# Optimization experiments

Hardware: AMD Instinct MI355X
Metric: run time of the kernel (lower is better)

Reference implementation:

```python
import jax, jax.numpy as jnp
import numpy as np

ALPHA = 1e-4
BETA = 1.0
MAX_STD = 1000.0
MIN_STD = 1.0
B = 8192            # number of ragged segments (batch)
NUM_CLASSES = 2
P = 1_000_000       # size of penalized parameter vector


def setup_inputs() -> dict:
    key = jax.random.key(0)
    k1, k2, k3, k4 = jax.random.split(key, 4)
    # ragged lengths: alternate 1024 / 3072, exact total T = B * 2048
    lengths = np.where(np.arange(B) % 2 == 0, 1024, 3072).astype(np.int32)
    T = int(lengths.sum())  # 16_777_216
    seg = np.repeat(np.arange(B, dtype=np.int32), lengths)
    starts = np.concatenate([[0], np.cumsum(lengths)[:-1]])
    local = np.arange(T, dtype=np.int64) - np.repeat(starts, lengths)
    # get_x: positions (1..len)/len within each segment
    xpos = ((local + 1).astype(np.float64) / np.repeat(lengths, lengths)).astype(np.float32)
    return {
        "logits": jax.random.normal(k1, (B, NUM_CLASSES), jnp.float32),
        "labels": jax.random.randint(k2, (B,), 0, 2, jnp.int32),
        "attention_weights": jax.random.uniform(k3, (T,), jnp.float32),
        "params": jax.random.normal(k4, (P,), jnp.float32),
        "xpos": jnp.asarray(xpos),
        "segment_ids": jnp.asarray(seg),
        "lengths": jnp.asarray(lengths),
    }


def reference(logits, labels, attention_weights, params, xpos, segment_ids, lengths):
    nseg = logits.shape[0]
    lens_f = lengths.astype(jnp.float32)

    # CrossEntropyLoss (mean reduction)
    logp = jax.nn.log_softmax(logits, axis=-1)
    nll = -jnp.mean(jnp.take_along_axis(logp, labels[:, None].astype(jnp.int32), axis=1))

    # --- no-grad block: per-segment mean and ideal-gaussian target r ---
    w = jax.lax.stop_gradient(attention_weights)
    sum_w = jax.ops.segment_sum(w, segment_ids, num_segments=nseg)          # [B]
    mean = jax.ops.segment_sum(xpos * w, segment_ids, num_segments=nseg) / sum_w
    ideal_std = jnp.where(labels == 1, MIN_STD, MAX_STD) / lens_f           # [B]
    mu_t = mean[segment_ids]                                                # [T]
    std_t = ideal_std[segment_ids]                                          # [T]
    z = (xpos - mu_t) / std_t
    r_hat = jnp.exp(-0.5 * z * z) / (std_t * jnp.sqrt(2.0 * jnp.pi))        # normal pdf
    r_sum = jax.ops.segment_sum(r_hat, segment_ids, num_segments=nseg)
    r = r_hat / (r_sum[segment_ids] + 1e-6)
    r = jax.lax.stop_gradient(r)

    # L1 penalty on params
    penalty = ALPHA / 2 * jnp.abs(params).sum()

    # per-segment mean of squared diff, then mean over segments
    diff2 = (attention_weights - r) ** 2
    per_seg = jax.ops.segment_sum(diff2, segment_ids, num_segments=nseg) / lens_f
    awp = BETA / 2 * per_seg.mean()

    loss = nll + penalty + awp
    return jnp.stack([loss, nll])
```

## Files before the change

kernel.cpp:

```cpp
#include <hip/hip_runtime.h>


#define TPB 256
#define PARAM_BLOCKS 256
#define SEGS_PER_BLOCK 4

__device__ __forceinline__ void waveReduce3(float& a, float& b, float& c) {
  #pragma unroll
  for (int off = 32; off > 0; off >>= 1) {
    a += __shfl_xor(a, off, 64);
    b += __shfl_xor(b, off, 64);
    c += __shfl_xor(c, off, 64);
  }
}

__device__ __forceinline__ float blockReduceSum(float v, float* sm) {
  #pragma unroll
  for (int off = 32; off > 0; off >>= 1) v += __shfl_down(v, off, 64);
  const int lane = threadIdx.x & 63;
  const int wid  = threadIdx.x >> 6;
  if (lane == 0) sm[wid] = v;
  __syncthreads();
  float s = sm[0] + sm[1] + sm[2] + sm[3];
  __syncthreads();
  return s;
}

__global__ __launch_bounds__(TPB)
void scan_kernel(const int* __restrict__ lengths, int nseg,
                 int* __restrict__ starts) {
  __shared__ int wsum[4];
  const int t = threadIdx.x;
  const int per = (nseg + TPB - 1) / TPB;
  const int base = t * per;
  int local = 0;
  for (int j = 0; j < per; j++) {
    int idx = base + j;
    if (idx < nseg) local += lengths[idx];
  }
  const int lane = t & 63, wid = t >> 6;
  int incl = local;
  #pragma unroll
  for (int off = 1; off < 64; off <<= 1) {
    int n = __shfl_up(incl, off, 64);
    if (lane >= off) incl += n;
  }
  if (lane == 63) wsum[wid] = incl;
  __syncthreads();
  int wbase = 0;
  for (int i = 0; i < wid; i++) wbase += wsum[i];
  int run = wbase + incl - local;
  for (int j = 0; j < per; j++) {
    int idx = base + j;
    if (idx < nseg) { starts[idx] = run; run += lengths[idx]; }
  }
}

template <int NC>
__device__ __forceinline__ float seg_wave(const float4* __restrict__ w4,
                                          int start4, int len, int lab) {
  const int lane = threadIdx.x & 63;
  const float inv_len = 1.0f / (float)len;
  float4 wv[NC];
  float aw = 0.0f, axw = 0.0f, aww = 0.0f;
  #pragma unroll
  for (int k = 0; k < NC; k++) {
    const int vi = (k << 6) + lane;
    wv[k] = w4[start4 + vi];
    const int i0 = vi << 2;
    aw += wv[k].x + wv[k].y + wv[k].z + wv[k].w;
    axw = fmaf((float)(i0 + 1) * inv_len, wv[k].x, axw);
    axw = fmaf((float)(i0 + 2) * inv_len, wv[k].y, axw);
    axw = fmaf((float)(i0 + 3) * inv_len, wv[k].z, axw);
    axw = fmaf((float)(i0 + 4) * inv_len, wv[k].w, axw);
    aww = fmaf(wv[k].x, wv[k].x, aww);
    aww = fmaf(wv[k].y, wv[k].y, aww);
    aww = fmaf(wv[k].z, wv[k].z, aww);
    aww = fmaf(wv[k].w, wv[k].w, aww);
  }
  waveReduce3(aw, axw, aww);
  const float mean = axw / aw;
  const float invstd = (float)len * (lab == 1 ? 1.0f : 0.001f);
  const float rn = 0.39894228040143267f * invstd;
  float ar = 0.0f, awr = 0.0f, arr = 0.0f;
  #pragma unroll
  for (int k = 0; k < NC; k++) {
    const int i0 = ((k << 6) + lane) << 2;
    float z0 = ((float)(i0 + 1) * inv_len - mean) * invstd;
    float z1 = ((float)(i0 + 2) * inv_len - mean) * invstd;
    float z2 = ((float)(i0 + 3) * inv_len - mean) * invstd;
    float z3 = ((float)(i0 + 4) * inv_len - mean) * invstd;
    float r0 = __expf(-0.5f * z0 * z0) * rn;
    float r1 = __expf(-0.5f * z1 * z1) * rn;
    float r2 = __expf(-0.5f * z2 * z2) * rn;
    float r3 = __expf(-0.5f * z3 * z3) * rn;
    ar += r0 + r1 + r2 + r3;
    awr = fmaf(wv[k].x, r0, awr); awr = fmaf(wv[k].y, r1, awr);
    awr = fmaf(wv[k].z, r2, awr); awr = fmaf(wv[k].w, r3, awr);
    arr = fmaf(r0, r0, arr); arr = fmaf(r1, r1, arr);
    arr = fmaf(r2, r2, arr); arr = fmaf(r3, r3, arr);
  }
  waveReduce3(ar, awr, arr);
  const float rinv = 1.0f / (ar + 1e-6f);
  const float dsum = aww - 2.0f * rinv * awr + rinv * rinv * arr;
  return dsum * inv_len;
}

__device__ float seg_wave_generic(const float* __restrict__ w, int start,
                                  int len, int lab) {
  const int lane = threadIdx.x & 63;
  const float inv_len = 1.0f / (float)len;
  float aw = 0.0f, axw = 0.0f, aww = 0.0f;
  for (int i = lane; i < len; i += 64) {
    float wv = w[start + i];
    aw += wv;
    axw = fmaf((float)(i + 1) * inv_len, wv, axw);
    aww = fmaf(wv, wv, aww);
  }
  waveReduce3(aw, axw, aww);
  const float mean = axw / aw;
  const float invstd = (float)len * (lab == 1 ? 1.0f : 0.001f);
  const float rn = 0.39894228040143267f * invstd;
  float ar = 0.0f, awr = 0.0f, arr = 0.0f;
  for (int i = lane; i < len; i += 64) {
    float z = ((float)(i + 1) * inv_len - mean) * invstd;
    float rh = __expf(-0.5f * z * z) * rn;
    ar += rh;
    awr = fmaf(w[start + i], rh, awr);
    arr = fmaf(rh, rh, arr);
  }
  waveReduce3(ar, awr, arr);
  const float rinv = 1.0f / (ar + 1e-6f);
  const float dsum = aww - 2.0f * rinv * awr + rinv * rinv * arr;
  return dsum * inv_len;
}

__global__ __launch_bounds__(TPB)
void main_kernel(const float* __restrict__ attw, const float* __restrict__ params,
                 const float* __restrict__ logits, const int* __restrict__ labels,
                 const int* __restrict__ lengths, const int* __restrict__ starts,
                 int nseg, int P, float* __restrict__ partial) {
  __shared__ float sm[4];
  const int b = blockIdx.x;
  const int nsegblk = (nseg + SEGS_PER_BLOCK - 1) / SEGS_PER_BLOCK;
  if (b < nsegblk) {
    const int wid = threadIdx.x >> 6;
    const int seg = b * SEGS_PER_BLOCK + wid;
    if (seg < nseg) {
      const int len = lengths[seg];
      const int start = starts[seg];
      const int lab = labels[seg];
      float r;
      if (len == 1024 && (start & 3) == 0)
        r = seg_wave<4>((const float4*)attw, start >> 2, len, lab);
      else if (len == 3072 && (start & 3) == 0)
        r = seg_wave<12>((const float4*)attw, start >> 2, len, lab);
      else
        r = seg_wave_generic(attw, start, len, lab);
      if ((threadIdx.x & 63) == 0) partial[seg] = r;
    }
  } else if (b < nsegblk + PARAM_BLOCKS) {
    const int pb = b - nsegblk;
    const int P4 = P >> 2;
    const float4* p4 = (const float4*)params;
    float a = 0.0f;
    for (int i = pb * TPB + threadIdx.x; i < P4; i += PARAM_BLOCKS * TPB) {
      float4 v = p4[i];
      a += fabsf(v.x) + fabsf(v.y) + fabsf(v.z) + fabsf(v.w);
    }
    if (pb == 0 && threadIdx.x == 0)
      for (int i = P4 << 2; i < P; i++) a += fabsf(params[i]);
    float tot = blockReduceSum(a, sm);
    if (threadIdx.x == 0) partial[nseg + pb] = tot;
  } else {
    float acc = 0.0f;
    for (int s = threadIdx.x; s < nseg; s += TPB) {
      float l0 = logits[2 * s], l1 = logits[2 * s + 1];
      int lab = labels[s];
      float m = fmaxf(l0, l1);
      float lse = m + logf(expf(l0 - m) + expf(l1 - m));
      acc += (lab ? l1 : l0) - lse;
    }
    float tot = blockReduceSum(acc, sm);
    if (threadIdx.x == 0) partial[nseg + PARAM_BLOCKS] = tot;
  }
}

__global__ __launch_bounds__(TPB)
void finalize_kernel(const float* __restrict__ partial, int nseg,
                     float* __restrict__ out) {
  __shared__ float sm[8];
  float a_awp = 0.0f, a_abs = 0.0f;
  for (int i = threadIdx.x; i < nseg; i += TPB) a_awp += partial[i];
  for (int i = threadIdx.x; i < PARAM_BLOCKS; i += TPB) a_abs += partial[nseg + i];
  #pragma unroll
  for (int off = 32; off > 0; off >>= 1) {
    a_awp += __shfl_down(a_awp, off, 64);
    a_abs += __shfl_down(a_abs, off, 64);
  }
  const int lane = threadIdx.x & 63, wid = threadIdx.x >> 6;
  if (lane == 0) { sm[wid] = a_awp; sm[4 + wid] = a_abs; }
  __syncthreads();
  if (threadIdx.x == 0) {
    float s_awp = sm[0] + sm[1] + sm[2] + sm[3];
    float s_abs = sm[4] + sm[5] + sm[6] + sm[7];
    const float nll = -partial[nseg + PARAM_BLOCKS] / (float)nseg;
    const float penalty = 0.5f * 1e-4f * s_abs;
    const float awp = 0.5f * (s_awp / (float)nseg);
    out[0] = nll + penalty + awp;
    out[1] = nll;
  }
}

extern "C" void kernel_launch(void* const* d_in, const int* in_sizes, int n_in,
                              void* d_out, int out_size, void* d_ws, size_t ws_size,
                              hipStream_t stream) {
  const float* logits  = (const float*)d_in[0];
  const int*   labels  = (const int*)d_in[1];
  const float* attw    = (const float*)d_in[2];
  const float* params  = (const float*)d_in[3];
  const int*   lengths = (const int*)d_in[6];
  const int nseg = in_sizes[1];
  const int P    = in_sizes[3];

  int* starts = (int*)d_ws;
  size_t poff = ((size_t)nseg * sizeof(int) + 255) & ~(size_t)255;
  float* partial = (float*)((char*)d_ws + poff);
  float* out = (float*)d_out;

  const int nsegblk = (nseg + SEGS_PER_BLOCK - 1) / SEGS_PER_BLOCK;
  scan_kernel<<<1, TPB, 0, stream>>>(lengths, nseg, starts);
  main_kernel<<<nsegblk + PARAM_BLOCKS + 1, TPB, 0, stream>>>(
      attw, params, logits, labels, lengths, starts, nseg, P, partial);
  finalize_kernel<<<1, TPB, 0, stream>>>(partial, nseg, out);
}
```

Baseline: 211.3 us.

## Assign one block per segment instead of one wave per segment

Each segment is now processed by a full 256-thread block instead of a single 64-lane wave. Every wave partial is combined through shared memory, and each thread holds 1 or 3 float4 values rather than 4 or 12. The goal is to balance load between short and long segments, cut register pressure and give the memory system more parallelism. The z computation is also folded into a single FMA with precomputed constants. In exchange the kernel adds block barriers and launches four times as many blocks.

```diff
diff --git a/kernel.cpp b/kernel.cpp
--- a/kernel.cpp
+++ b/kernel.cpp
@@ -3,27 +3,30 @@
 
 #define TPB 256
 #define PARAM_BLOCKS 256
-#define SEGS_PER_BLOCK 4
-
-__device__ __forceinline__ void waveReduce3(float& a, float& b, float& c) {
+
+__device__ __forceinline__ void blockReduce3(float& a, float& b, float& c,
+                                             float* sm) {
   #pragma unroll
   for (int off = 32; off > 0; off >>= 1) {
     a += __shfl_xor(a, off, 64);
     b += __shfl_xor(b, off, 64);
     c += __shfl_xor(c, off, 64);
   }
+  const int lane = threadIdx.x & 63, wid = threadIdx.x >> 6;
+  if (lane == 0) { sm[wid] = a; sm[4 + wid] = b; sm[8 + wid] = c; }
+  __syncthreads();
+  a = sm[0] + sm[1] + sm[2] + sm[3];
+  b = sm[4] + sm[5] + sm[6] + sm[7];
+  c = sm[8] + sm[9] + sm[10] + sm[11];
 }
 
 __device__ __forceinline__ float blockReduceSum(float v, float* sm) {
   #pragma unroll
-  for (int off = 32; off > 0; off >>= 1) v += __shfl_down(v, off, 64);
-  const int lane = threadIdx.x & 63;
-  const int wid  = threadIdx.x >> 6;
+  for (int off = 32; off > 0; off >>= 1) v += __shfl_xor(v, off, 64);
+  const int lane = threadIdx.x & 63, wid = threadIdx.x >> 6;
   if (lane == 0) sm[wid] = v;
   __syncthreads();
-  float s = sm[0] + sm[1] + sm[2] + sm[3];
-  __syncthreads();
-  return s;
+  return sm[0] + sm[1] + sm[2] + sm[3];
 }
 
 __global__ __launch_bounds__(TPB)
@@ -57,15 +60,15 @@
 }
 
 template <int NC>
-__device__ __forceinline__ float seg_wave(const float4* __restrict__ w4,
-                                          int start4, int len, int lab) {
-  const int lane = threadIdx.x & 63;
+__device__ __forceinline__ float seg_body(const float4* __restrict__ w4,
+                                          int start4, int len, int lab,
+                                          float* sm) {
   const float inv_len = 1.0f / (float)len;
   float4 wv[NC];
   float aw = 0.0f, axw = 0.0f, aww = 0.0f;
   #pragma unroll
   for (int k = 0; k < NC; k++) {
-    const int vi = (k << 6) + lane;
+    const int vi = (k << 8) + threadIdx.x;
     wv[k] = w4[start4 + vi];
     const int i0 = vi << 2;
     aw += wv[k].x + wv[k].y + wv[k].z + wv[k].w;
@@ -78,18 +81,20 @@
     aww = fmaf(wv[k].z, wv[k].z, aww);
     aww = fmaf(wv[k].w, wv[k].w, aww);
   }
-  waveReduce3(aw, axw, aww);
+  blockReduce3(aw, axw, aww, sm);
   const float mean = axw / aw;
   const float invstd = (float)len * (lab == 1 ? 1.0f : 0.001f);
   const float rn = 0.39894228040143267f * invstd;
+  const float c1 = inv_len * invstd;
+  const float m2 = mean * invstd;
   float ar = 0.0f, awr = 0.0f, arr = 0.0f;
   #pragma unroll
   for (int k = 0; k < NC; k++) {
-    const int i0 = ((k << 6) + lane) << 2;
-    float z0 = ((float)(i0 + 1) * inv_len - mean) * invstd;
-    float z1 = ((float)(i0 + 2) * inv_len - mean) * invstd;
-    float z2 = ((float)(i0 + 3) * inv_len - mean) * invstd;
-    float z3 = ((float)(i0 + 4) * inv_len - mean) * invstd;
+    const int i0 = (((k << 8) + threadIdx.x)) << 2;
+    float z0 = fmaf((float)(i0 + 1), c1, -m2);
+    float z1 = fmaf((float)(i0 + 2), c1, -m2);
+    float z2 = fmaf((float)(i0 + 3), c1, -m2);
+    float z3 = fmaf((float)(i0 + 4), c1, -m2);
     float r0 = __expf(-0.5f * z0 * z0) * rn;
     float r1 = __expf(-0.5f * z1 * z1) * rn;
     float r2 = __expf(-0.5f * z2 * z2) * rn;
@@ -100,36 +105,35 @@
     arr = fmaf(r0, r0, arr); arr = fmaf(r1, r1, arr);
     arr = fmaf(r2, r2, arr); arr = fmaf(r3, r3, arr);
   }
-  waveReduce3(ar, awr, arr);
+  blockReduce3(ar, awr, arr, sm + 12);
   const float rinv = 1.0f / (ar + 1e-6f);
   const float dsum = aww - 2.0f * rinv * awr + rinv * rinv * arr;
   return dsum * inv_len;
 }
 
-__device__ float seg_wave_generic(const float* __restrict__ w, int start,
-                                  int len, int lab) {
-  const int lane = threadIdx.x & 63;
+__device__ float seg_generic(const float* __restrict__ w, int start, int len,
+                             int lab, float* sm) {
   const float inv_len = 1.0f / (float)len;
   float aw = 0.0f, axw = 0.0f, aww = 0.0f;
-  for (int i = lane; i < len; i += 64) {
+  for (int i = threadIdx.x; i < len; i += TPB) {
     float wv = w[start + i];
     aw += wv;
     axw = fmaf((float)(i + 1) * inv_len, wv, axw);
     aww = fmaf(wv, wv, aww);
   }
-  waveReduce3(aw, axw, aww);
+  blockReduce3(aw, axw, aww, sm);
   const float mean = axw / aw;
   const float invstd = (float)len * (lab == 1 ? 1.0f : 0.001f);
   const float rn = 0.39894228040143267f * invstd;
   float ar = 0.0f, awr = 0.0f, arr = 0.0f;
-  for (int i = lane; i < len; i += 64) {
+  for (int i = threadIdx.x; i < len; i += TPB) {
     float z = ((float)(i + 1) * inv_len - mean) * invstd;
     float rh = __expf(-0.5f * z * z) * rn;
     ar += rh;
     awr = fmaf(w[start + i], rh, awr);
     arr = fmaf(rh, rh, arr);
   }
-  waveReduce3(ar, awr, arr);
+  blockReduce3(ar, awr, arr, sm + 12);
   const float rinv = 1.0f / (ar + 1e-6f);
   const float dsum = aww - 2.0f * rinv * awr + rinv * rinv * arr;
   return dsum * inv_len;
@@ -140,27 +144,22 @@
                  const float* __restrict__ logits, const int* __restrict__ labels,
                  const int* __restrict__ lengths, const int* __restrict__ starts,
                  int nseg, int P, float* __restrict__ partial) {
-  __shared__ float sm[4];
+  __shared__ float sm[24];
   const int b = blockIdx.x;
-  const int nsegblk = (nseg + SEGS_PER_BLOCK - 1) / SEGS_PER_BLOCK;
-  if (b < nsegblk) {
-    const int wid = threadIdx.x >> 6;
-    const int seg = b * SEGS_PER_BLOCK + wid;
-    if (seg < nseg) {
-      const int len = lengths[seg];
-      const int start = starts[seg];
-      const int lab = labels[seg];
-      float r;
-      if (len == 1024 && (start & 3) == 0)
-        r = seg_wave<4>((const float4*)attw, start >> 2, len, lab);
-      else if (len == 3072 && (start & 3) == 0)
-        r = seg_wave<12>((const float4*)attw, start >> 2, len, lab);
-      else
-        r = seg_wave_generic(attw, start, len, lab);
-      if ((threadIdx.x & 63) == 0) partial[seg] = r;
-    }
-  } else if (b < nsegblk + PARAM_BLOCKS) {
-    const int pb = b - nsegblk;
+  if (b < nseg) {
+    const int len = lengths[b];
+    const int start = starts[b];
+    const int lab = labels[b];
+    float r;
+    if (len == 1024 && (start & 3) == 0)
+      r = seg_body<1>((const float4*)attw, start >> 2, len, lab, sm);
+    else if (len == 3072 && (start & 3) == 0)
+      r = seg_body<3>((const float4*)attw, start >> 2, len, lab, sm);
+    else
+      r = seg_generic(attw, start, len, lab, sm);
+    if (threadIdx.x == 0) partial[b] = r;
+  } else if (b < nseg + PARAM_BLOCKS) {
+    const int pb = b - nseg;
     const int P4 = P >> 2;
     const float4* p4 = (const float4*)params;
     float a = 0.0f;
@@ -195,8 +194,8 @@
   for (int i = threadIdx.x; i < PARAM_BLOCKS; i += TPB) a_abs += partial[nseg + i];
   #pragma unroll
   for (int off = 32; off > 0; off >>= 1) {
-    a_awp += __shfl_down(a_awp, off, 64);
-    a_abs += __shfl_down(a_abs, off, 64);
+    a_awp += __shfl_xor(a_awp, off, 64);
+    a_abs += __shfl_xor(a_abs, off, 64);
   }
   const int lane = threadIdx.x & 63, wid = threadIdx.x >> 6;
   if (lane == 0) { sm[wid] = a_awp; sm[4 + wid] = a_abs; }
@@ -228,9 +227,8 @@
   float* partial = (float*)((char*)d_ws + poff);
   float* out = (float*)d_out;
 
-  const int nsegblk = (nseg + SEGS_PER_BLOCK - 1) / SEGS_PER_BLOCK;
   scan_kernel<<<1, TPB, 0, stream>>>(lengths, nseg, starts);
-  main_kernel<<<nsegblk + PARAM_BLOCKS + 1, TPB, 0, stream>>>(
+  main_kernel<<<nseg + PARAM_BLOCKS + 1, TPB, 0, stream>>>(
       attw, params, logits, labels, lengths, starts, nseg, P, partial);
   finalize_kernel<<<1, TPB, 0, stream>>>(partial, nseg, out);
 }
```

Result: no change. 210.5 us (-0.4%).
